# Optimization experiments

Measured on AMD Instinct MI355X. Metric: run time of the kernel, lower is better.

Reference implementation:

```python
import jax, jax.numpy as jnp
import numpy as np
import math

B, N, C = 4, 8192, 384
H = 6
D = C // H  # head_dim = 64


def setup_inputs() -> dict:
    key = jax.random.key(0)
    ks = jax.random.split(key, 9)
    s = 1.0 / math.sqrt(D)
    x = jax.random.normal(ks[0], (B, N, C), dtype=jnp.float32)
    Wq = jax.random.normal(ks[1], (H, D, D), dtype=jnp.float32) * s
    bq = jax.random.normal(ks[2], (H, D), dtype=jnp.float32) * 0.01
    Wk = jax.random.normal(ks[3], (H, D, D), dtype=jnp.float32) * s
    bk = jax.random.normal(ks[4], (H, D), dtype=jnp.float32) * 0.01
    Wv = jax.random.normal(ks[5], (H, D, D), dtype=jnp.float32) * s
    bv = jax.random.normal(ks[6], (H, D), dtype=jnp.float32) * 0.01
    Wp = jax.random.normal(ks[7], (C, C), dtype=jnp.float32) * (1.0 / math.sqrt(C))
    bp = jax.random.normal(ks[8], (C,), dtype=jnp.float32) * 0.01
    return {"x": x, "Wq": Wq, "bq": bq, "Wk": Wk, "bk": bk,
            "Wv": Wv, "bv": bv, "Wp": Wp, "bp": bp}


def reference(x, Wq, bq, Wk, bk, Wv, bv, Wp, bp):
    b, n, c = x.shape
    # [B, H, N, D]
    xh = x.reshape(b, n, H, D).transpose(0, 2, 1, 3)
    # Batched per-head projections (replaces the Python loop of per-head Linears)
    q = jnp.einsum('bhnd,hde->bhne', xh, Wq) + bq[:, None, :]
    k = jnp.einsum('bhnd,hde->bhne', xh, Wk) + bk[:, None, :]
    v = jnp.einsum('bhnd,hde->bhne', xh, Wv) + bv[:, None, :]
    q = jax.nn.softmax(q, axis=-1)          # over feature dim
    k = jax.nn.softmax(k, axis=-2)          # over sequence dim
    v = v * (1.0 / math.sqrt(D))
    kv = jnp.einsum('bhnd,bhne->bhde', k, v)   # [B,H,D,D] context
    out = jnp.einsum('bhnd,bhde->bhne', q, kv) # [B,H,N,D]
    out = out.transpose(0, 2, 1, 3).reshape(b, n, c)
    return out @ Wp.T + bp
```

## Files before the change

### kernel.cpp

```cpp
#include <hip/hip_runtime.h>
#include <hip/hip_bf16.h>


#define B 4
#define N 8192
#define C 384
#define H 6
#define D 64
#define BH (B * H)
#define BN (B * N)

typedef __attribute__((ext_vector_type(8))) short short8;
typedef __attribute__((ext_vector_type(4))) float f32x4;

__device__ inline unsigned short f2bf(float f) {
    unsigned int u = __float_as_uint(f);
    unsigned int r = (u + 0x7fff + ((u >> 16) & 1)) >> 16;
    return (unsigned short)r;
}

__global__ void wprep(const float* __restrict__ Wq, const float* __restrict__ Wk,
                      const float* __restrict__ Wv, unsigned short* __restrict__ Wt)
{
    __shared__ float tmp[64][65];
    const int m = blockIdx.x / H;
    const int h = blockIdx.x % H;
    const float* in = (m == 0 ? Wq : m == 1 ? Wk : Wv) + h * 64 * 64;
    const int t = threadIdx.x;
    for (int d = 0; d < 64; ++d) tmp[d][t] = in[d * 64 + t];
    __syncthreads();
    const size_t base = ((size_t)(m * H + h)) * 64 * 64;
    for (int e = 0; e < 64; ++e)
        Wt[base + e * 64 + t] = f2bf(tmp[t][e]);
}

__global__ __launch_bounds__(256, 2) void proj_kernel(
    const float* __restrict__ x, const unsigned short* __restrict__ Wt,
    const float* __restrict__ bq, const float* __restrict__ bk,
    const float* __restrict__ bv,
    unsigned short* __restrict__ qout,
    float* __restrict__ kvraw, float* __restrict__ Sg)
{
    __shared__ __align__(16) char smem[34816];
    unsigned short* W_s = (unsigned short*)smem;
    unsigned short* qbuf = (unsigned short*)(smem + 24576);
    float* kvred = (float*)smem;
    float* sred  = (float*)(smem + 33792);

    const int blk = blockIdx.x;
    const int nb  = blk & 31;
    const int bh  = blk >> 5;
    const int b   = bh / H;
    const int h   = bh % H;
    const int n0  = nb * 256;
    const int t   = threadIdx.x;
    const int lane = t & 63;
    const int w   = t >> 6;
    const int lq  = lane & 15;
    const int qd  = lane >> 4;

    {
        const size_t hb = (size_t)h * 4096;
        for (int id = t; id < 512; id += 256) {
            int e = id >> 3, c = id & 7;
            int dc = ((c ^ (e & 7)) * 8);
            #pragma unroll
            for (int m = 0; m < 3; ++m)
                *(uint4*)&W_s[m * 4096 + e * 64 + dc] =
                    *(const uint4*)(Wt + (size_t)m * H * 4096 + hb + e * 64 + c * 8);
        }
    }

    float bqv[4], bkv[4], bvv[4];
    #pragma unroll
    for (int j = 0; j < 4; ++j) {
        int col = j * 16 + lq;
        bqv[j] = bq[h * D + col];
        bkv[j] = bk[h * D + col];
        bvv[j] = bv[h * D + col];
    }

    unsigned short* qw = qbuf + w * 1152;

    __syncthreads();

    f32x4 kvacc[4][4] = {};
    float sacc[4] = {};

    for (int sub = 0; sub < 4; ++sub) {
        const int ns = n0 + sub * 64;

        const float* ap = x + (size_t)(b * N + ns + w * 16 + lq) * C + h * D + qd * 8;
        short8 af[2];
        {
            float av[16];
            *(float4*)&av[0]  = *(const float4*)ap;
            *(float4*)&av[4]  = *(const float4*)(ap + 4);
            *(float4*)&av[8]  = *(const float4*)(ap + 32);
            *(float4*)&av[12] = *(const float4*)(ap + 36);
            #pragma unroll
            for (int ck = 0; ck < 2; ++ck)
                #pragma unroll
                for (int i = 0; i < 8; ++i)
                    af[ck][i] = (short)f2bf(av[ck * 8 + i]);
        }

        {
            f32x4 acc[4] = {};
            #pragma unroll
            for (int ck = 0; ck < 2; ++ck)
                #pragma unroll
                for (int j = 0; j < 4; ++j) {
                    const int pc = ((ck * 4 + qd) ^ (lq & 7)) * 8;
                    short8 bw = *(const short8*)&W_s[(j * 16 + lq) * 64 + pc];
                    acc[j] = __builtin_amdgcn_mfma_f32_16x16x32_bf16(af[ck], bw, acc[j], 0, 0, 0);
                }
            #pragma unroll
            for (int r = 0; r < 4; ++r) {
                float qv[4];
                #pragma unroll
                for (int j = 0; j < 4; ++j) qv[j] = acc[j][r] + bqv[j];
                float mx = fmaxf(fmaxf(qv[0], qv[1]), fmaxf(qv[2], qv[3]));
                #pragma unroll
                for (int msk = 1; msk < 16; msk <<= 1) mx = fmaxf(mx, __shfl_xor(mx, msk));
                float e0 = __expf(qv[0] - mx), e1 = __expf(qv[1] - mx);
                float e2 = __expf(qv[2] - mx), e3 = __expf(qv[3] - mx);
                float s = e0 + e1 + e2 + e3;
                #pragma unroll
                for (int msk = 1; msk < 16; msk <<= 1) s += __shfl_xor(s, msk);
                float inv = 1.f / s;
                const int row = qd * 4 + r;
                qw[row * 72 + 0 * 16 + lq] = f2bf(e0 * inv);
                qw[row * 72 + 1 * 16 + lq] = f2bf(e1 * inv);
                qw[row * 72 + 2 * 16 + lq] = f2bf(e2 * inv);
                qw[row * 72 + 3 * 16 + lq] = f2bf(e3 * inv);
            }
            const size_t gbase = (size_t)bh * N + ns + w * 16;
            #pragma unroll
            for (int rep = 0; rep < 2; ++rep) {
                int flat = rep * 64 + lane;
                int row = flat >> 3, c8 = flat & 7;
                *(uint4*)&qout[(gbase + row) * 64 + c8 * 8] =
                    *(uint4*)&qw[row * 72 + c8 * 8];
            }
        }
        __builtin_amdgcn_sched_barrier(0);

        short8 kfrag[4];
        {
            f32x4 acc[4] = {};
            #pragma unroll
            for (int ck = 0; ck < 2; ++ck)
                #pragma unroll
                for (int j = 0; j < 4; ++j) {
                    const int pc = ((ck * 4 + qd) ^ (lq & 7)) * 8;
                    short8 bw = *(const short8*)&W_s[4096 + (j * 16 + lq) * 64 + pc];
                    acc[j] = __builtin_amdgcn_mfma_f32_16x16x32_bf16(af[ck], bw, acc[j], 0, 0, 0);
                }
            #pragma unroll
            for (int j = 0; j < 4; ++j) {
                float e0 = __expf(acc[j][0] + bkv[j]);
                float e1 = __expf(acc[j][1] + bkv[j]);
                float e2 = __expf(acc[j][2] + bkv[j]);
                float e3 = __expf(acc[j][3] + bkv[j]);
                float cs = e0 + e1 + e2 + e3;
                cs += __shfl_xor(cs, 16);
                cs += __shfl_xor(cs, 32);
                sacc[j] += cs;
                kfrag[j] = short8{(short)f2bf(e0), (short)f2bf(e1),
                                  (short)f2bf(e2), (short)f2bf(e3), 0, 0, 0, 0};
            }
        }
        __builtin_amdgcn_sched_barrier(0);

        {
            f32x4 acc[4] = {};
            #pragma unroll
            for (int ck = 0; ck < 2; ++ck)
                #pragma unroll
                for (int j = 0; j < 4; ++j) {
                    const int pc = ((ck * 4 + qd) ^ (lq & 7)) * 8;
                    short8 bw = *(const short8*)&W_s[2 * 4096 + (j * 16 + lq) * 64 + pc];
                    acc[j] = __builtin_amdgcn_mfma_f32_16x16x32_bf16(af[ck], bw, acc[j], 0, 0, 0);
                }
            short8 vfrag[4];
            #pragma unroll
            for (int j = 0; j < 4; ++j) {
                float v0 = (acc[j][0] + bvv[j]) * 0.125f;
                float v1 = (acc[j][1] + bvv[j]) * 0.125f;
                float v2 = (acc[j][2] + bvv[j]) * 0.125f;
                float v3 = (acc[j][3] + bvv[j]) * 0.125f;
                vfrag[j] = short8{(short)f2bf(v0), (short)f2bf(v1),
                                  (short)f2bf(v2), (short)f2bf(v3), 0, 0, 0, 0};
            }
            #pragma unroll
            for (int i = 0; i < 4; ++i)
                #pragma unroll
                for (int j = 0; j < 4; ++j)
                    kvacc[i][j] = __builtin_amdgcn_mfma_f32_16x16x32_bf16(
                        kfrag[i], vfrag[j], kvacc[i][j], 0, 0, 0);
        }
        __builtin_amdgcn_sched_barrier(0);
    }

    __syncthreads();

    #pragma unroll
    for (int half = 0; half < 2; ++half) {
        #pragma unroll
        for (int i2 = 0; i2 < 2; ++i2) {
            const int ii = half * 2 + i2;
            #pragma unroll
            for (int j = 0; j < 4; ++j)
                #pragma unroll
                for (int r = 0; r < 4; ++r)
                    kvred[w * 2112 + (i2 * 16 + qd * 4 + r) * 66 + j * 16 + lq] =
                        kvacc[ii][j][r];
        }
        if (half == 0 && qd == 0) {
            #pragma unroll
            for (int j = 0; j < 4; ++j) sred[w * 64 + j * 16 + lq] = sacc[j];
        }
        __syncthreads();
        for (int idx = t; idx < 2048; idx += 256) {
            int dl = idx >> 6, e = idx & 63;
            float s = kvred[dl * 66 + e] + kvred[2112 + dl * 66 + e]
                    + kvred[2 * 2112 + dl * 66 + e] + kvred[3 * 2112 + dl * 66 + e];
            atomicAdd(&kvraw[bh * 4096 + (half * 32 + dl) * 64 + e], s);
        }
        if (half == 1 && t < 64) {
            float s = sred[t] + sred[64 + t] + sred[128 + t] + sred[192 + t];
            atomicAdd(&Sg[bh * 64 + t], s);
        }
        if (half == 0) __syncthreads();
    }
}

__global__ __launch_bounds__(256) void kw_kernel(
    const float* __restrict__ kvraw, const float* __restrict__ Sg,
    const float* __restrict__ Wp, unsigned short* __restrict__ KWT)
{
    __shared__ float kv_s[64 * 68];
    __shared__ float w_s[64 * 68];
    __shared__ float rS_s[64];
    const int bh = blockIdx.x / (C / 64);
    const int ct = blockIdx.x % (C / 64);
    const int b = bh / H, h = bh % H;
    const int c0 = ct * 64;
    const int t = threadIdx.x, dg = t >> 4, cg = t & 15;

    if (t < 64) rS_s[t] = 1.f / Sg[bh * 64 + t];
    __syncthreads();

    for (int i = t; i < 4096; i += 256) {
        int row = i >> 6, e = i & 63;
        kv_s[e * 68 + row] = kvraw[bh * (D * D) + row * 64 + e] * rS_s[row];
        w_s[e * 68 + row]  = Wp[(size_t)(c0 + row) * C + h * 64 + e];
    }
    __syncthreads();

    float acc[4][4] = {};
    for (int e = 0; e < 64; ++e) {
        float4 a = *(float4*)&kv_s[e * 68 + dg * 4];
        float4 w = *(float4*)&w_s[e * 68 + cg * 4];
        const float a4[4] = {a.x, a.y, a.z, a.w};
        const float w4[4] = {w.x, w.y, w.z, w.w};
        #pragma unroll
        for (int i = 0; i < 4; ++i)
            #pragma unroll
            for (int j = 0; j < 4; ++j) acc[i][j] += a4[i] * w4[j];
    }
    #pragma unroll
    for (int i = 0; i < 4; ++i)
        #pragma unroll
        for (int j = 0; j < 4; ++j) {
            int d = dg * 4 + i, c = c0 + cg * 4 + j;
            KWT[((size_t)b * C + c) * (H * D) + h * 64 + d] = f2bf(acc[i][j]);
        }
}

__global__ __launch_bounds__(256) void out_gemm(
    const unsigned short* __restrict__ q, const unsigned short* __restrict__ KWT,
    const float* __restrict__ bp, float* __restrict__ out)
{
    __shared__ __align__(16) unsigned short A_s[128 * 72];
    __shared__ __align__(16) unsigned short B_s[128 * 72];

    const int mt = blockIdx.x / (C / 128);
    const int ct = blockIdx.x % (C / 128);
    const int m0 = mt * 128, c0 = ct * 128;
    const int b  = m0 >> 13;
    const int n0 = m0 & (N - 1);
    const int t  = threadIdx.x;
    const int lane = t & 63;
    const int w  = t >> 6;
    const int wm = w >> 1, wn = w & 1;
    const int lq = lane & 15;
    const int qd = lane >> 4;

    f32x4 acc[4][4] = {};

    for (int h = 0; h < H; ++h) {
        if (h) __syncthreads();
        const unsigned short* qb = q + (size_t)(b * H + h) * N * D + (size_t)n0 * D;
        const unsigned short* kb = KWT + ((size_t)b * C + c0) * (H * D) + h * 64;
        #pragma unroll
        for (int it = 0; it < 4; ++it) {
            int id = it * 256 + t;
            int r = id >> 3, c8 = id & 7;
            *(uint4*)&A_s[r * 72 + c8 * 8] = *(const uint4*)(qb + r * 64 + c8 * 8);
            *(uint4*)&B_s[r * 72 + c8 * 8] = *(const uint4*)(kb + (size_t)r * (H * D) + c8 * 8);
        }
        __syncthreads();

        #pragma unroll
        for (int kk = 0; kk < 64; kk += 32) {
            short8 af[4], bf[4];
            #pragma unroll
            for (int i = 0; i < 4; ++i)
                af[i] = *(short8*)&A_s[(wm * 64 + i * 16 + lq) * 72 + kk + qd * 8];
            #pragma unroll
            for (int j = 0; j < 4; ++j)
                bf[j] = *(short8*)&B_s[(wn * 64 + j * 16 + lq) * 72 + kk + qd * 8];
            #pragma unroll
            for (int i = 0; i < 4; ++i)
                #pragma unroll
                for (int j = 0; j < 4; ++j)
                    acc[i][j] = __builtin_amdgcn_mfma_f32_16x16x32_bf16(
                        af[i], bf[j], acc[i][j], 0, 0, 0);
        }
    }

    float bpv[4];
    #pragma unroll
    for (int j = 0; j < 4; ++j) bpv[j] = bp[c0 + wn * 64 + j * 16 + lq];

    #pragma unroll
    for (int i = 0; i < 4; ++i) {
        #pragma unroll
        for (int r = 0; r < 4; ++r) {
            size_t row = (size_t)m0 + wm * 64 + i * 16 + qd * 4 + r;
            float* orow = out + row * C + c0 + wn * 64;
            #pragma unroll
            for (int j = 0; j < 4; ++j)
                orow[j * 16 + lq] = acc[i][j][r] + bpv[j];
        }
    }
}

extern "C" void kernel_launch(void* const* d_in, const int* in_sizes, int n_in,
                              void* d_out, int out_size, void* d_ws, size_t ws_size,
                              hipStream_t stream)
{
    const float* x  = (const float*)d_in[0];
    const float* Wq = (const float*)d_in[1];
    const float* bq = (const float*)d_in[2];
    const float* Wk = (const float*)d_in[3];
    const float* bk = (const float*)d_in[4];
    const float* Wv = (const float*)d_in[5];
    const float* bv = (const float*)d_in[6];
    const float* Wp = (const float*)d_in[7];
    const float* bp = (const float*)d_in[8];
    float* out = (float*)d_out;

    const size_t SZ = (size_t)B * H * N * D;
    float* ws   = (float*)d_ws;
    unsigned short* q = (unsigned short*)ws;
    float* kvraw = ws + SZ;
    float* Sg    = kvraw + (size_t)BH * D * D;
    unsigned short* KWT = (unsigned short*)(Sg + BH * 64);
    unsigned short* Wt  = KWT + (size_t)B * C * (H * D);

    wprep<<<3 * H, 64, 0, stream>>>(Wq, Wk, Wv, Wt);
    hipMemsetAsync(kvraw, 0, ((size_t)BH * D * D + BH * 64) * sizeof(float), stream);
    proj_kernel<<<BH * (N / 256), 256, 0, stream>>>(x, Wt, bq, bk, bv,
                                                    q, kvraw, Sg);
    kw_kernel<<<BH * (C / 64), 256, 0, stream>>>(kvraw, Sg, Wp, KWT);
    out_gemm<<<(BN / 128) * (C / 128), 256, 0, stream>>>(q, KWT, bp, out);
}
```

Before: 158.3 us.

## Pack bf16 conversions, drop q softmax max, prefetch out_gemm tiles, swizzle blocks

Replaces scalar bf16 rounding with the packed v_cvt_pk_bf16_f32 instruction, and removes the max-subtraction in the feature softmax, using a fast reciprocal instead. In out_gemm, the next head's q and KWT tiles are prefetched into registers while the current head's MFMAs run, and block indices are regrouped so neighbouring blocks share row tiles. Dropping the max is only safe while the logits stay small, and the prefetch raises register pressure.

```diff
diff --git a/kernel.cpp b/kernel.cpp
--- a/kernel.cpp
+++ b/kernel.cpp
@@ -17,6 +17,12 @@
     unsigned int u = __float_as_uint(f);
     unsigned int r = (u + 0x7fff + ((u >> 16) & 1)) >> 16;
     return (unsigned short)r;
+}
+
+__device__ inline unsigned int cvt2bf(float a, float b) {
+    unsigned int r;
+    asm("v_cvt_pk_bf16_f32 %0, %1, %2" : "=v"(r) : "v"(a), "v"(b));
+    return r;
 }
 
 __global__ void wprep(const float* __restrict__ Wq, const float* __restrict__ Wk,
@@ -98,11 +104,10 @@
             *(float4*)&av[4]  = *(const float4*)(ap + 4);
             *(float4*)&av[8]  = *(const float4*)(ap + 32);
             *(float4*)&av[12] = *(const float4*)(ap + 36);
-            #pragma unroll
-            for (int ck = 0; ck < 2; ++ck)
-                #pragma unroll
-                for (int i = 0; i < 8; ++i)
-                    af[ck][i] = (short)f2bf(av[ck * 8 + i]);
+            unsigned int* afu = (unsigned int*)af;
+            #pragma unroll
+            for (int p = 0; p < 8; ++p)
+                afu[p] = cvt2bf(av[2 * p], av[2 * p + 1]);
         }
 
         {
@@ -117,23 +122,21 @@
                 }
             #pragma unroll
             for (int r = 0; r < 4; ++r) {
-                float qv[4];
-                #pragma unroll
-                for (int j = 0; j < 4; ++j) qv[j] = acc[j][r] + bqv[j];
-                float mx = fmaxf(fmaxf(qv[0], qv[1]), fmaxf(qv[2], qv[3]));
-                #pragma unroll
-                for (int msk = 1; msk < 16; msk <<= 1) mx = fmaxf(mx, __shfl_xor(mx, msk));
-                float e0 = __expf(qv[0] - mx), e1 = __expf(qv[1] - mx);
-                float e2 = __expf(qv[2] - mx), e3 = __expf(qv[3] - mx);
-                float s = e0 + e1 + e2 + e3;
+                float e0 = __expf(acc[0][r] + bqv[0]);
+                float e1 = __expf(acc[1][r] + bqv[1]);
+                float e2 = __expf(acc[2][r] + bqv[2]);
+                float e3 = __expf(acc[3][r] + bqv[3]);
+                float s = (e0 + e1) + (e2 + e3);
                 #pragma unroll
                 for (int msk = 1; msk < 16; msk <<= 1) s += __shfl_xor(s, msk);
-                float inv = 1.f / s;
+                float inv = __builtin_amdgcn_rcpf(s);
+                unsigned int p01 = cvt2bf(e0 * inv, e1 * inv);
+                unsigned int p23 = cvt2bf(e2 * inv, e3 * inv);
                 const int row = qd * 4 + r;
-                qw[row * 72 + 0 * 16 + lq] = f2bf(e0 * inv);
-                qw[row * 72 + 1 * 16 + lq] = f2bf(e1 * inv);
-                qw[row * 72 + 2 * 16 + lq] = f2bf(e2 * inv);
-                qw[row * 72 + 3 * 16 + lq] = f2bf(e3 * inv);
+                qw[row * 72 + 0 * 16 + lq] = (unsigned short)p01;
+                qw[row * 72 + 1 * 16 + lq] = (unsigned short)(p01 >> 16);
+                qw[row * 72 + 2 * 16 + lq] = (unsigned short)p23;
+                qw[row * 72 + 3 * 16 + lq] = (unsigned short)(p23 >> 16);
             }
             const size_t gbase = (size_t)bh * N + ns + w * 16;
             #pragma unroll
@@ -163,12 +166,15 @@
                 float e1 = __expf(acc[j][1] + bkv[j]);
                 float e2 = __expf(acc[j][2] + bkv[j]);
                 float e3 = __expf(acc[j][3] + bkv[j]);
-                float cs = e0 + e1 + e2 + e3;
+                float cs = (e0 + e1) + (e2 + e3);
                 cs += __shfl_xor(cs, 16);
                 cs += __shfl_xor(cs, 32);
                 sacc[j] += cs;
-                kfrag[j] = short8{(short)f2bf(e0), (short)f2bf(e1),
-                                  (short)f2bf(e2), (short)f2bf(e3), 0, 0, 0, 0};
+                unsigned int* kf = (unsigned int*)&kfrag[j];
+                kf[0] = cvt2bf(e0, e1);
+                kf[1] = cvt2bf(e2, e3);
+                kf[2] = 0;
+                kf[3] = 0;
             }
         }
         __builtin_amdgcn_sched_barrier(0);
@@ -190,8 +196,11 @@
                 float v1 = (acc[j][1] + bvv[j]) * 0.125f;
                 float v2 = (acc[j][2] + bvv[j]) * 0.125f;
                 float v3 = (acc[j][3] + bvv[j]) * 0.125f;
-                vfrag[j] = short8{(short)f2bf(v0), (short)f2bf(v1),
-                                  (short)f2bf(v2), (short)f2bf(v3), 0, 0, 0, 0};
+                unsigned int* vf = (unsigned int*)&vfrag[j];
+                vf[0] = cvt2bf(v0, v1);
+                vf[1] = cvt2bf(v2, v3);
+                vf[2] = 0;
+                vf[3] = 0;
             }
             #pragma unroll
             for (int i = 0; i < 4; ++i)
@@ -286,8 +295,11 @@
     __shared__ __align__(16) unsigned short A_s[128 * 72];
     __shared__ __align__(16) unsigned short B_s[128 * 72];
 
-    const int mt = blockIdx.x / (C / 128);
-    const int ct = blockIdx.x % (C / 128);
+    const int bid = blockIdx.x;
+    const int grp = bid / 24;
+    const int rem = bid % 24;
+    const int ct  = rem >> 3;
+    const int mt  = grp * 8 + (rem & 7);
     const int m0 = mt * 128, c0 = ct * 128;
     const int b  = m0 >> 13;
     const int n0 = m0 & (N - 1);
@@ -299,19 +311,40 @@
     const int qd = lane >> 4;
 
     f32x4 acc[4][4] = {};
+    uint4 pa[4], pb[4];
+
+    const int sid = t;
+    const int sr  = sid >> 3, sc8 = sid & 7;
+
+    {
+        const unsigned short* qb = q + (size_t)(b * H + 0) * N * D + (size_t)n0 * D;
+        const unsigned short* kb = KWT + ((size_t)b * C + c0) * (H * D) + 0 * 64;
+        #pragma unroll
+        for (int it = 0; it < 4; ++it) {
+            int r = sr + it * 32;
+            pa[it] = *(const uint4*)(qb + r * 64 + sc8 * 8);
+            pb[it] = *(const uint4*)(kb + (size_t)r * (H * D) + sc8 * 8);
+        }
+        #pragma unroll
+        for (int it = 0; it < 4; ++it) {
+            int r = sr + it * 32;
+            *(uint4*)&A_s[r * 72 + sc8 * 8] = pa[it];
+            *(uint4*)&B_s[r * 72 + sc8 * 8] = pb[it];
+        }
+    }
+    __syncthreads();
 
     for (int h = 0; h < H; ++h) {
-        if (h) __syncthreads();
-        const unsigned short* qb = q + (size_t)(b * H + h) * N * D + (size_t)n0 * D;
-        const unsigned short* kb = KWT + ((size_t)b * C + c0) * (H * D) + h * 64;
-        #pragma unroll
-        for (int it = 0; it < 4; ++it) {
-            int id = it * 256 + t;
-            int r = id >> 3, c8 = id & 7;
-            *(uint4*)&A_s[r * 72 + c8 * 8] = *(const uint4*)(qb + r * 64 + c8 * 8);
-            *(uint4*)&B_s[r * 72 + c8 * 8] = *(const uint4*)(kb + (size_t)r * (H * D) + c8 * 8);
-        }
-        __syncthreads();
+        if (h + 1 < H) {
+            const unsigned short* qb = q + (size_t)(b * H + h + 1) * N * D + (size_t)n0 * D;
+            const unsigned short* kb = KWT + ((size_t)b * C + c0) * (H * D) + (h + 1) * 64;
+            #pragma unroll
+            for (int it = 0; it < 4; ++it) {
+                int r = sr + it * 32;
+                pa[it] = *(const uint4*)(qb + r * 64 + sc8 * 8);
+                pb[it] = *(const uint4*)(kb + (size_t)r * (H * D) + sc8 * 8);
+            }
+        }
 
         #pragma unroll
         for (int kk = 0; kk < 64; kk += 32) {
@@ -328,6 +361,17 @@
                 for (int j = 0; j < 4; ++j)
                     acc[i][j] = __builtin_amdgcn_mfma_f32_16x16x32_bf16(
                         af[i], bf[j], acc[i][j], 0, 0, 0);
+        }
+
+        __syncthreads();
+        if (h + 1 < H) {
+            #pragma unroll
+            for (int it = 0; it < 4; ++it) {
+                int r = sr + it * 32;
+                *(uint4*)&A_s[r * 72 + sc8 * 8] = pa[it];
+                *(uint4*)&B_s[r * 72 + sc8 * 8] = pb[it];
+            }
+            __syncthreads();
         }
     }
 
```

Result: slower. 186.9 us (+18.1%).
